# Kernel optimization log

Hardware: AMD Instinct MI355X
Metric: run time of the kernel (lower is better)

Reference implementation:

```python
import jax, jax.numpy as jnp
import numpy as np

D_MODEL = 1024
N_HEADS = 16
D_K = D_MODEL // N_HEADS
ROPE_THETA = 10000.0


def setup_inputs() -> dict:
    key = jax.random.key(0)
    ks = jax.random.split(key, 5)
    B, S = 2, 2048
    scale = 1.0 / np.sqrt(D_MODEL)
    return {
        "x": jax.random.normal(ks[0], (B, S, D_MODEL), dtype=jnp.float32),
        "token_positions": jnp.arange(S, dtype=jnp.int32),
        "Wq": jax.random.normal(ks[1], (D_MODEL, D_MODEL), dtype=jnp.float32) * scale,
        "Wk": jax.random.normal(ks[2], (D_MODEL, D_MODEL), dtype=jnp.float32) * scale,
        "Wv": jax.random.normal(ks[3], (D_MODEL, D_MODEL), dtype=jnp.float32) * scale,
        "Wo": jax.random.normal(ks[4], (D_MODEL, D_MODEL), dtype=jnp.float32) * scale,
    }


def apply_rope(x, positions):
    # x: [b, h, s, d_k]; interleaved-pair rotary embedding, theta=10000
    half = D_K // 2
    inv_freq = ROPE_THETA ** (-jnp.arange(0, half, dtype=x.dtype) * 2.0 / D_K)  # [half]
    angles = positions.astype(x.dtype)[:, None] * inv_freq[None, :]             # [s, half]
    cos, sin = jnp.cos(angles), jnp.sin(angles)                                 # [s, half]
    x1 = x[..., 0::2]
    x2 = x[..., 1::2]
    r1 = x1 * cos - x2 * sin
    r2 = x1 * sin + x2 * cos
    # re-interleave
    return jnp.stack([r1, r2], axis=-1).reshape(x.shape)


def reference(x, token_positions, Wq, Wk, Wv, Wo):
    B, S, _ = x.shape
    # Linear(d_model, d_model) with no bias: y = x @ W.T
    Q = jnp.einsum("bsd,ed->bse", x, Wq).reshape(B, S, N_HEADS, D_K).transpose(0, 2, 1, 3)
    K = jnp.einsum("bsd,ed->bse", x, Wk).reshape(B, S, N_HEADS, D_K).transpose(0, 2, 1, 3)
    V = jnp.einsum("bsd,ed->bse", x, Wv).reshape(B, S, N_HEADS, D_K).transpose(0, 2, 1, 3)
    Q = apply_rope(Q, token_positions)
    K = apply_rope(K, token_positions)
    scores = jnp.einsum("bhqd,bhkd->bhqk", Q, K) / jnp.sqrt(jnp.asarray(D_K, x.dtype))
    causal = jnp.tril(jnp.ones((S, S), dtype=bool))
    scores = jnp.where(causal[None, None, :, :], scores, jnp.asarray(-jnp.inf, x.dtype))
    attn = jax.nn.softmax(scores, axis=-1)
    out = jnp.einsum("bhqk,bhkd->bhqd", attn, V)            # [b, h, s, d_k]
    out = out.transpose(0, 2, 1, 3).reshape(B, S, D_MODEL)   # [b, s, d_model]
    return jnp.einsum("bsd,ed->bse", out, Wo)
```

## Files before the change

### kernel.cpp

```cpp
#include <hip/hip_runtime.h>
#include <hip/hip_bf16.h>
#include <math.h>

#define SEQ 2048
#define NH  16
#define DKH 64
#define DM  1024
#define MR  4096

using bf16x8 = __attribute__((ext_vector_type(8))) short;
using f32x4  = __attribute__((ext_vector_type(4))) float;
using f32x16 = __attribute__((ext_vector_type(16))) float;

__device__ __forceinline__ ushort f2b(float f) {
  unsigned u = __float_as_uint(f);
  return (ushort)((u + 0x7fffu + ((u >> 16) & 1u)) >> 16);
}

__device__ __forceinline__ float exp2_fast(float x) {
  float r; asm("v_exp_f32 %0, %1" : "=v"(r) : "v"(x)); return r;
}

__device__ __forceinline__ unsigned cvt_pk(float lo, float hi) {
  __hip_bfloat162 h = __float22bfloat162_rn(float2{lo, hi});
  return *reinterpret_cast<unsigned*>(&h);
}

__device__ __forceinline__ float xhalf_max(float x) {
  auto r = __builtin_amdgcn_permlane32_swap(__float_as_uint(x), __float_as_uint(x), false, false);
  return fmaxf(__uint_as_float(r[0]), __uint_as_float(r[1]));
}
__device__ __forceinline__ float xhalf_add(float x) {
  auto r = __builtin_amdgcn_permlane32_swap(__float_as_uint(x), __float_as_uint(x), false, false);
  return __uint_as_float(r[0]) + __uint_as_float(r[1]);
}

__device__ __forceinline__ void gll16(const void* g, void* l) {
  __builtin_amdgcn_global_load_lds(
      (const __attribute__((address_space(1))) void*)g,
      (__attribute__((address_space(3))) void*)l, 16, 0, 0);
}

__global__ __launch_bounds__(256) void cvt_all(
    const float* __restrict__ x,  const float* __restrict__ wq,
    const float* __restrict__ wk, const float* __restrict__ wv,
    const float* __restrict__ wo,
    ushort* __restrict__ xb,  ushort* __restrict__ wqb, ushort* __restrict__ wkb,
    ushort* __restrict__ wvb, ushort* __restrict__ wob)
{
  size_t e = ((size_t)blockIdx.x * 256 + threadIdx.x) * 4;
  const float* s; ushort* d; size_t off;
  if      (e < 4194304) { s = x;  d = xb;  off = e; }
  else if (e < 5242880) { s = wq; d = wqb; off = e - 4194304; }
  else if (e < 6291456) { s = wk; d = wkb; off = e - 5242880; }
  else if (e < 7340032) { s = wv; d = wvb; off = e - 6291456; }
  else                  { s = wo; d = wob; off = e - 7340032; }
  float4 f = *(const float4*)(s + off);
  ushort4 o4 = { f2b(f.x), f2b(f.y), f2b(f.z), f2b(f.w) };
  *(ushort4*)(d + off) = o4;
}

__global__ __launch_bounds__(512) void gemm_qkv(
    const ushort* __restrict__ X,
    const ushort* __restrict__ Wq, const ushort* __restrict__ Wk, const ushort* __restrict__ Wv,
    ushort* __restrict__ Q, ushort* __restrict__ K, ushort* __restrict__ Vt,
    const int* __restrict__ pos)
{
  __shared__ __align__(16) char As[2][16384];
  __shared__ __align__(16) char Bs[2][16384];

  const int id  = blockIdx.x;
  const int xcd = id & 7;
  const int i   = id >> 3;
  const int mt  = xcd * 4 + (i & 3);
  const int nt  = i >> 2;
  const int m0  = mt * 128;
  const int nG  = nt * 128;
  const int z   = nG >> 10;
  const int n0  = nG & 1023;
  const ushort* W = (z == 0) ? Wq : (z == 1) ? Wk : Wv;

  const int tid  = threadIdx.x;
  const int lane = tid & 63;
  const int w    = tid >> 6;
  const int wm   = (w >> 2) * 64;
  const int wn   = (w & 3) * 32;
  const int li   = lane & 15;
  const int g    = lane >> 4;

  f32x4 acc[4][2] = {};

  auto stage = [&](int t, int buf) {
    const int k0 = t * 64;
    #pragma unroll
    for (int it = 0; it < 2; ++it) {
      const int L  = w * 2048 + it * 1024 + lane * 16;
      const int r  = L >> 7;
      const int sc = ((L >> 4) & 7) ^ (r & 7);
      gll16(X + (size_t)(m0 + r) * DM + k0 + sc * 8, &As[buf][w * 2048 + it * 1024]);
      gll16(W + (size_t)(n0 + r) * DM + k0 + sc * 8, &Bs[buf][w * 2048 + it * 1024]);
    }
  };

  auto compute = [&](int buf) {
    #pragma unroll
    for (int ks = 0; ks < 2; ++ks) {
      bf16x8 af[4], bfr[2];
      #pragma unroll
      for (int mf = 0; mf < 4; ++mf) {
        const int row = wm + mf * 16 + li;
        af[mf] = *(const bf16x8*)(&As[buf][row * 128 + (((ks * 4 + g) ^ (row & 7)) << 4)]);
      }
      #pragma unroll
      for (int nf = 0; nf < 2; ++nf) {
        const int row = wn + nf * 16 + li;
        bfr[nf] = *(const bf16x8*)(&Bs[buf][row * 128 + (((ks * 4 + g) ^ (row & 7)) << 4)]);
      }
      #pragma unroll
      for (int mf = 0; mf < 4; ++mf)
        #pragma unroll
        for (int nf = 0; nf < 2; ++nf)
          acc[mf][nf] = __builtin_amdgcn_mfma_f32_16x16x32_bf16(af[mf], bfr[nf], acc[mf][nf], 0, 0, 0);
    }
  };

  stage(0, 0);
  for (int t = 0; t < 16; ++t) {
    if (t < 15) {
      stage(t + 1, (t + 1) & 1);
      __builtin_amdgcn_sched_barrier(0);
      asm volatile("s_waitcnt vmcnt(4)" ::: "memory");
    } else {
      asm volatile("s_waitcnt vmcnt(0)" ::: "memory");
    }
    __builtin_amdgcn_s_barrier();
    __builtin_amdgcn_sched_barrier(0);
    compute(t & 1);
    __builtin_amdgcn_sched_barrier(0);
    __builtin_amdgcn_s_barrier();
  }

  #pragma unroll
  for (int nf = 0; nf < 2; ++nf) {
    const int n = n0 + wn + nf * 16 + li;
    const int h = n >> 6;
    const int d = n & 63;
    if (z == 2) {
      #pragma unroll
      for (int mf = 0; mf < 4; ++mf) {
        const int m  = m0 + wm + mf * 16 + g * 4;
        const int b  = m >> 11;
        const int s2 = m & (SEQ - 1);
        ushort4 pk = { f2b(acc[mf][nf][0]), f2b(acc[mf][nf][1]),
                       f2b(acc[mf][nf][2]), f2b(acc[mf][nf][3]) };
        *(ushort4*)(Vt + (((size_t)b * NH + h) * DKH + d) * SEQ + s2) = pk;
      }
    } else {
      ushort* DST = (z == 0) ? Q : K;
      const float freq = __expf(-(float)(d >> 1) * 0.2878231366242557f);
      #pragma unroll
      for (int mf = 0; mf < 4; ++mf) {
        #pragma unroll
        for (int r = 0; r < 4; ++r) {
          const int m  = m0 + wm + mf * 16 + g * 4 + r;
          const int b  = m >> 11;
          const int s2 = m & (SEQ - 1);
          const float ang = (float)pos[s2] * freq;
          float sn, cs;
          __sincosf(ang, &sn, &cs);
          const float v1 = acc[mf][nf][r];
          const float v2 = __shfl_xor(v1, 1);
          float ov = (d & 1) ? (v2 * sn + v1 * cs)
                             : (v1 * cs - v2 * sn);
          if (z == 0) ov *= 0.1803368801111204f;
          DST[(((size_t)b * NH + h) * SEQ + s2) * DKH + d] = f2b(ov);
        }
      }
    }
  }
}

__global__ __launch_bounds__(512) void gemm_wo(
    const ushort* __restrict__ A, const ushort* __restrict__ W,
    float* __restrict__ out)
{
  __shared__ __align__(16) char As[2][16384];
  __shared__ __align__(16) char Bs[2][16384];

  const int id  = blockIdx.x;
  const int xcd = id & 7;
  const int i   = id >> 3;
  const int mt  = xcd * 4 + (i & 3);
  const int nt  = i >> 2;
  const int m0  = mt * 128;
  const int n0  = nt * 128;

  const int tid  = threadIdx.x;
  const int lane = tid & 63;
  const int w    = tid >> 6;
  const int wm   = (w >> 2) * 64;
  const int wn   = (w & 3) * 32;
  const int li   = lane & 15;
  const int g    = lane >> 4;

  f32x4 acc[4][2] = {};

  auto stage = [&](int t, int buf) {
    const int k0 = t * 64;
    #pragma unroll
    for (int it = 0; it < 2; ++it) {
      const int L  = w * 2048 + it * 1024 + lane * 16;
      const int r  = L >> 7;
      const int sc = ((L >> 4) & 7) ^ (r & 7);
      gll16(A + (size_t)(m0 + r) * DM + k0 + sc * 8, &As[buf][w * 2048 + it * 1024]);
      gll16(W + (size_t)(n0 + r) * DM + k0 + sc * 8, &Bs[buf][w * 2048 + it * 1024]);
    }
  };

  auto compute = [&](int buf) {
    #pragma unroll
    for (int ks = 0; ks < 2; ++ks) {
      bf16x8 af[4], bfr[2];
      #pragma unroll
      for (int mf = 0; mf < 4; ++mf) {
        const int row = wm + mf * 16 + li;
        af[mf] = *(const bf16x8*)(&As[buf][row * 128 + (((ks * 4 + g) ^ (row & 7)) << 4)]);
      }
      #pragma unroll
      for (int nf = 0; nf < 2; ++nf) {
        const int row = wn + nf * 16 + li;
        bfr[nf] = *(const bf16x8*)(&Bs[buf][row * 128 + (((ks * 4 + g) ^ (row & 7)) << 4)]);
      }
      #pragma unroll
      for (int mf = 0; mf < 4; ++mf)
        #pragma unroll
        for (int nf = 0; nf < 2; ++nf)
          acc[mf][nf] = __builtin_amdgcn_mfma_f32_16x16x32_bf16(af[mf], bfr[nf], acc[mf][nf], 0, 0, 0);
    }
  };

  stage(0, 0);
  for (int t = 0; t < 16; ++t) {
    if (t < 15) {
      stage(t + 1, (t + 1) & 1);
      __builtin_amdgcn_sched_barrier(0);
      asm volatile("s_waitcnt vmcnt(4)" ::: "memory");
    } else {
      asm volatile("s_waitcnt vmcnt(0)" ::: "memory");
    }
    __builtin_amdgcn_s_barrier();
    __builtin_amdgcn_sched_barrier(0);
    compute(t & 1);
    __builtin_amdgcn_sched_barrier(0);
    __builtin_amdgcn_s_barrier();
  }

  #pragma unroll
  for (int nf = 0; nf < 2; ++nf)
    #pragma unroll
    for (int mf = 0; mf < 4; ++mf)
      #pragma unroll
      for (int r = 0; r < 4; ++r)
        out[(size_t)(m0 + wm + mf * 16 + g * 4 + r) * DM + n0 + wn + nf * 16 + li] = acc[mf][nf][r];
}

__global__ __launch_bounds__(256) void attn(
    const ushort* __restrict__ Q, const ushort* __restrict__ K,
    const ushort* __restrict__ Vt, ushort* __restrict__ AO)
{
  __shared__ __align__(16) char KsB[2][8192];
  __shared__ __align__(16) char VsB[2][8192];

  const int tid  = threadIdx.x;
  const int lane = tid & 63;
  const int w    = tid >> 6;
  const int lq   = lane & 31;
  const int hi   = lane >> 5;

  const int bx  = blockIdx.x;
  const int xcd = bx & 7;
  const int idx = bx >> 3;
  int u, s;
  if (idx < 32) { u = 15 - (idx >> 1); s = idx & 1; }
  else          { u = (idx - 32) >> 1; s = 2 + ((idx - 32) & 1); }
  const int bh   = s * 8 + xcd;
  const int ntr  = 2 * u + 2;
  const int q0w  = u * 128 + w * 32;
  const int q_abs = q0w + lq;
  const int t_max = (q0w + 31) >> 6;

  const ushort* Qb = Q  + (size_t)bh * SEQ * DKH;
  const ushort* Kb = K  + (size_t)bh * SEQ * DKH;
  const ushort* Vb = Vt + (size_t)bh * DKH * SEQ;

  bf16x8 qf[4];
  #pragma unroll
  for (int db = 0; db < 4; ++db)
    qf[db] = *(const bf16x8*)(Qb + (size_t)(q0w + lq) * DKH + db * 16 + hi * 8);

  f32x16 o0 = {}, o1 = {};
  float m_ = -INFINITY, l_ = 0.f;

  auto stage = [&](int kt, int buf) {
    const int k0 = kt * 64;
    #pragma unroll
    for (int it = 0; it < 2; ++it) {
      const int L  = w * 2048 + it * 1024 + lane * 16;
      const int r  = L >> 7;
      const int sc = ((L >> 4) & 7) ^ (r & 7);
      gll16(Kb + (size_t)(k0 + r) * DKH + sc * 8, &KsB[buf][w * 2048 + it * 1024]);
      gll16(Vb + (size_t)r * SEQ + k0 + sc * 8,   &VsB[buf][w * 2048 + it * 1024]);
    }
  };

#define PVSTEP(P, S4) do {                                                   \
    unsigned A0 = cvt_pk((P)[((S4)&1)*8 + 0], (P)[((S4)&1)*8 + 1]);          \
    unsigned A1 = cvt_pk((P)[((S4)&1)*8 + 2], (P)[((S4)&1)*8 + 3]);          \
    unsigned B0 = cvt_pk((P)[((S4)&1)*8 + 4], (P)[((S4)&1)*8 + 5]);          \
    unsigned B1 = cvt_pk((P)[((S4)&1)*8 + 6], (P)[((S4)&1)*8 + 7]);          \
    auto r0 = __builtin_amdgcn_permlane32_swap(A0, B0, false, false);        \
    auto r1 = __builtin_amdgcn_permlane32_swap(A1, B1, false, false);        \
    int4 ti = { (int)r0[0], (int)r1[0], (int)r0[1], (int)r1[1] };            \
    bf16x8 pf = *(bf16x8*)&ti;                                               \
    const int uv = (S4) * 2 + hi;                                            \
    bf16x8 va = *(const bf16x8*)(Vc + lq * 128      + ((uv ^ (lq & 7)) << 4)); \
    bf16x8 vb = *(const bf16x8*)(Vc + (32+lq) * 128 + ((uv ^ (lq & 7)) << 4)); \
    o0 = __builtin_amdgcn_mfma_f32_32x32x16_bf16(va, pf, o0, 0, 0, 0);       \
    o1 = __builtin_amdgcn_mfma_f32_32x32x16_bf16(vb, pf, o1, 0, 0, 0);       \
  } while (0)

  auto computeT = [&](int t, int buf, bool diag) {
    const char* Kc = KsB[buf];
    const char* Vc = VsB[buf];
    const int k0 = t * 64;

    f32x16 st0 = {}, st1 = {};
    __builtin_amdgcn_s_setprio(1);
    #pragma unroll
    for (int db = 0; db < 4; ++db) {
      const int uk = db * 2 + hi;
      bf16x8 ka = *(const bf16x8*)(Kc + lq * 128      + ((uk ^ (lq & 7)) << 4));
      bf16x8 kb = *(const bf16x8*)(Kc + (32+lq) * 128 + ((uk ^ (lq & 7)) << 4));
      st0 = __builtin_amdgcn_mfma_f32_32x32x16_bf16(ka, qf[db], st0, 0, 0, 0);
      st1 = __builtin_amdgcn_mfma_f32_32x32x16_bf16(kb, qf[db], st1, 0, 0, 0);
    }
    __builtin_amdgcn_s_setprio(0);

    if (diag) {
      #pragma unroll
      for (int reg = 0; reg < 16; ++reg) {
        const int kvr = (reg & 3) + 8 * (reg >> 2) + 4 * hi;
        if (k0 + kvr > q_abs)      st0[reg] = -1e30f;
        if (k0 + 32 + kvr > q_abs) st1[reg] = -1e30f;
      }
    }

    float mx = st0[0];
    #pragma unroll
    for (int r = 1; r < 16; ++r) mx = fmaxf(mx, st0[r]);
    #pragma unroll
    for (int r = 0; r < 16; ++r) mx = fmaxf(mx, st1[r]);
    mx = xhalf_max(mx);

    const bool resc = !__all(mx - m_ <= 8.0f);
    float al = 1.0f;
    if (resc) { const float nm = fmaxf(m_, mx); al = exp2_fast(m_ - nm); m_ = nm; }

    float rs = 0.f;
    #pragma unroll
    for (int r = 0; r < 16; ++r) { st0[r] = exp2_fast(st0[r] - m_); rs += st0[r]; }
    #pragma unroll
    for (int r = 0; r < 16; ++r) { st1[r] = exp2_fast(st1[r] - m_); rs += st1[r]; }
    rs = xhalf_add(rs);

    if (resc) {
      l_ = l_ * al + rs;
      #pragma unroll
      for (int r = 0; r < 16; ++r) { o0[r] *= al; o1[r] *= al; }
    } else {
      l_ += rs;
    }

    __builtin_amdgcn_s_setprio(1);
    PVSTEP(st0, 0);
    PVSTEP(st0, 1);
    PVSTEP(st1, 2);
    PVSTEP(st1, 3);
    __builtin_amdgcn_s_setprio(0);
  };

  stage(0, 0);
  for (int t = 0; t < ntr; ++t) {
    if (t + 1 < ntr) {
      stage(t + 1, (t + 1) & 1);
      __builtin_amdgcn_sched_barrier(0);
      asm volatile("s_waitcnt vmcnt(4)" ::: "memory");
    } else {
      asm volatile("s_waitcnt vmcnt(0)" ::: "memory");
    }
    __builtin_amdgcn_s_barrier();
    __builtin_amdgcn_sched_barrier(0);
    if (t <= t_max) computeT(t, t & 1, t == t_max);
    __builtin_amdgcn_sched_barrier(0);
    __builtin_amdgcn_s_barrier();
  }

  const float inv = 1.0f / l_;
  const int b = bh >> 4, h = bh & 15;
  ushort* dst = AO + ((size_t)b * SEQ + q_abs) * DM + h * DKH;

#define STORE16(OV, DSUB) do {                                               \
    _Pragma("unroll")                                                        \
    for (int rq = 0; rq < 4; ++rq) {                                         \
      const int d0 = (DSUB) * 32 + rq * 8 + hi * 4;                          \
      uint2 pk = { cvt_pk((OV)[rq*4+0] * inv, (OV)[rq*4+1] * inv),           \
                   cvt_pk((OV)[rq*4+2] * inv, (OV)[rq*4+3] * inv) };         \
      *(uint2*)(dst + d0) = pk;                                              \
    }                                                                        \
  } while (0)

  STORE16(o0, 0);
  STORE16(o1, 1);
}

extern "C" void kernel_launch(void* const* d_in, const int* in_sizes, int n_in,
                              void* d_out, int out_size, void* d_ws, size_t ws_size,
                              hipStream_t stream)
{
  const float* x   = (const float*)d_in[0];
  const int*   pos = (const int*)  d_in[1];
  const float* Wq  = (const float*)d_in[2];
  const float* Wk  = (const float*)d_in[3];
  const float* Wv  = (const float*)d_in[4];
  const float* Wo  = (const float*)d_in[5];
  float* out = (float*)d_out;

  ushort* ws  = (ushort*)d_ws;
  ushort* xb  = ws;
  ushort* wqb = xb  + 4194304;
  ushort* wkb = wqb + 1048576;
  ushort* wvb = wkb + 1048576;
  ushort* wob = wvb + 1048576;
  ushort* Qb  = wob + 1048576;
  ushort* Kb  = Qb  + 4194304;
  ushort* Vtb = Kb  + 4194304;
  ushort* AOb = Vtb + 4194304;

  cvt_all<<<8192, 256, 0, stream>>>(x, Wq, Wk, Wv, Wo, xb, wqb, wkb, wvb, wob);
  gemm_qkv<<<768, 512, 0, stream>>>(xb, wqb, wkb, wvb, Qb, Kb, Vtb, pos);
  attn<<<512, 256, 0, stream>>>(Qb, Kb, Vtb, AOb);
  gemm_wo<<<256, 512, 0, stream>>>(AOb, wob, out);
}
```

Before: 118.0 us.

## Split attention into single-wave blocks with per-wave KV staging, no double buffer

The attention kernel moves from 256-thread blocks, where four waves share double-buffered K/V tiles, to 64-thread single-wave blocks, each handling 32 query rows. Each block stages its own K/V tile synchronously before computing, so block barriers go away and causal work is balanced per wave, with heavier blocks scheduled first. The cost is that K/V is no longer shared across four waves, so global/L2 traffic grows about fourfold. The load-compute overlap is also lost, since each tile load is waited on in full before compute starts.

```diff
diff --git a/kernel.cpp b/kernel.cpp
--- a/kernel.cpp
+++ b/kernel.cpp
@@ -264,30 +264,25 @@
         out[(size_t)(m0 + wm + mf * 16 + g * 4 + r) * DM + n0 + wn + nf * 16 + li] = acc[mf][nf][r];
 }
 
-__global__ __launch_bounds__(256) void attn(
+__global__ __launch_bounds__(64) void attn(
     const ushort* __restrict__ Q, const ushort* __restrict__ K,
     const ushort* __restrict__ Vt, ushort* __restrict__ AO)
 {
-  __shared__ __align__(16) char KsB[2][8192];
-  __shared__ __align__(16) char VsB[2][8192];
-
-  const int tid  = threadIdx.x;
-  const int lane = tid & 63;
-  const int w    = tid >> 6;
+  __shared__ __align__(16) char Ks[8192];
+  __shared__ __align__(16) char Vs[8192];
+
+  const int lane = threadIdx.x & 63;
   const int lq   = lane & 31;
   const int hi   = lane >> 5;
 
   const int bx  = blockIdx.x;
   const int xcd = bx & 7;
-  const int idx = bx >> 3;
-  int u, s;
-  if (idx < 32) { u = 15 - (idx >> 1); s = idx & 1; }
-  else          { u = (idx - 32) >> 1; s = 2 + ((idx - 32) & 1); }
-  const int bh   = s * 8 + xcd;
-  const int ntr  = 2 * u + 2;
-  const int q0w  = u * 128 + w * 32;
+  const int i   = bx >> 3;
+  const int uu  = 63 - (i >> 2);
+  const int bh  = (i & 3) * 8 + xcd;
+  const int q0w = uu * 32;
+  const int ntr = (uu >> 1) + 1;
   const int q_abs = q0w + lq;
-  const int t_max = (q0w + 31) >> 6;
 
   const ushort* Qb = Q  + (size_t)bh * SEQ * DKH;
   const ushort* Kb = K  + (size_t)bh * SEQ * DKH;
@@ -301,15 +296,15 @@
   f32x16 o0 = {}, o1 = {};
   float m_ = -INFINITY, l_ = 0.f;
 
-  auto stage = [&](int kt, int buf) {
+  auto stage = [&](int kt) {
     const int k0 = kt * 64;
     #pragma unroll
-    for (int it = 0; it < 2; ++it) {
-      const int L  = w * 2048 + it * 1024 + lane * 16;
+    for (int it = 0; it < 8; ++it) {
+      const int L  = it * 1024 + lane * 16;
       const int r  = L >> 7;
       const int sc = ((L >> 4) & 7) ^ (r & 7);
-      gll16(Kb + (size_t)(k0 + r) * DKH + sc * 8, &KsB[buf][w * 2048 + it * 1024]);
-      gll16(Vb + (size_t)r * SEQ + k0 + sc * 8,   &VsB[buf][w * 2048 + it * 1024]);
+      gll16(Kb + (size_t)(k0 + r) * DKH + sc * 8, Ks + it * 1024);
+      gll16(Vb + (size_t)r * SEQ + k0 + sc * 8,   Vs + it * 1024);
     }
   };
 
@@ -323,15 +318,13 @@
     int4 ti = { (int)r0[0], (int)r1[0], (int)r0[1], (int)r1[1] };            \
     bf16x8 pf = *(bf16x8*)&ti;                                               \
     const int uv = (S4) * 2 + hi;                                            \
-    bf16x8 va = *(const bf16x8*)(Vc + lq * 128      + ((uv ^ (lq & 7)) << 4)); \
-    bf16x8 vb = *(const bf16x8*)(Vc + (32+lq) * 128 + ((uv ^ (lq & 7)) << 4)); \
+    bf16x8 va = *(const bf16x8*)(Vs + lq * 128      + ((uv ^ (lq & 7)) << 4)); \
+    bf16x8 vb = *(const bf16x8*)(Vs + (32+lq) * 128 + ((uv ^ (lq & 7)) << 4)); \
     o0 = __builtin_amdgcn_mfma_f32_32x32x16_bf16(va, pf, o0, 0, 0, 0);       \
     o1 = __builtin_amdgcn_mfma_f32_32x32x16_bf16(vb, pf, o1, 0, 0, 0);       \
   } while (0)
 
-  auto computeT = [&](int t, int buf, bool diag) {
-    const char* Kc = KsB[buf];
-    const char* Vc = VsB[buf];
+  auto computeT = [&](int t, bool diag) {
     const int k0 = t * 64;
 
     f32x16 st0 = {}, st1 = {};
@@ -339,8 +332,8 @@
     #pragma unroll
     for (int db = 0; db < 4; ++db) {
       const int uk = db * 2 + hi;
-      bf16x8 ka = *(const bf16x8*)(Kc + lq * 128      + ((uk ^ (lq & 7)) << 4));
-      bf16x8 kb = *(const bf16x8*)(Kc + (32+lq) * 128 + ((uk ^ (lq & 7)) << 4));
+      bf16x8 ka = *(const bf16x8*)(Ks + lq * 128      + ((uk ^ (lq & 7)) << 4));
+      bf16x8 kb = *(const bf16x8*)(Ks + (32+lq) * 128 + ((uk ^ (lq & 7)) << 4));
       st0 = __builtin_amdgcn_mfma_f32_32x32x16_bf16(ka, qf[db], st0, 0, 0, 0);
       st1 = __builtin_amdgcn_mfma_f32_32x32x16_bf16(kb, qf[db], st1, 0, 0, 0);
     }
@@ -389,20 +382,12 @@
     __builtin_amdgcn_s_setprio(0);
   };
 
-  stage(0, 0);
   for (int t = 0; t < ntr; ++t) {
-    if (t + 1 < ntr) {
-      stage(t + 1, (t + 1) & 1);
-      __builtin_amdgcn_sched_barrier(0);
-      asm volatile("s_waitcnt vmcnt(4)" ::: "memory");
-    } else {
-      asm volatile("s_waitcnt vmcnt(0)" ::: "memory");
-    }
-    __builtin_amdgcn_s_barrier();
-    __builtin_amdgcn_sched_barrier(0);
-    if (t <= t_max) computeT(t, t & 1, t == t_max);
-    __builtin_amdgcn_sched_barrier(0);
-    __builtin_amdgcn_s_barrier();
+    __builtin_amdgcn_sched_barrier(0);
+    stage(t);
+    __builtin_amdgcn_sched_barrier(0);
+    asm volatile("s_waitcnt vmcnt(0)" ::: "memory");
+    computeT(t, t == ntr - 1);
   }
 
   const float inv = 1.0f / l_;
@@ -448,6 +433,6 @@
 
   cvt_all<<<8192, 256, 0, stream>>>(x, Wq, Wk, Wv, Wo, xb, wqb, wkb, wvb, wob);
   gemm_qkv<<<768, 512, 0, stream>>>(xb, wqb, wkb, wvb, Qb, Kb, Vtb, pos);
-  attn<<<512, 256, 0, stream>>>(Qb, Kb, Vtb, AOb);
+  attn<<<2048, 64, 0, stream>>>(Qb, Kb, Vtb, AOb);
   gemm_wo<<<256, 512, 0, stream>>>(AOb, wob, out);
 }
```

Measured after the change: 113.2 us. 1.04x faster.
